# Kernel optimization log

Hardware: AMD Instinct MI355X
Metric: run time of the kernel (lower is better)

The kernel has to match this reference:

```python
import jax, jax.numpy as jnp
import numpy as np

_LARGE = 1e10
LN_EPS = 1e-12
K_TOP = 32
ROWS = 512


def setup_inputs() -> dict:
    key = jax.random.key(0)
    ks = jax.random.split(key, 12)
    B, T, H = 32, 128, 768
    M, D_KEY, D_VAL = 131072, 128, 512
    N = 1024  # n_mentions
    return {
        'encoding': jax.random.normal(ks[0], (B, T, H), jnp.float32),
        'mention_batch_positions': jax.random.randint(ks[1], (N,), 0, B),
        'mention_start_positions': jax.random.randint(ks[2], (N,), 0, T),
        'mention_end_positions': jax.random.randint(ks[3], (N,), 0, T),
        'mention_mask': jnp.ones((N,), jnp.float32),
        'memory_keys': jax.random.normal(ks[4], (M, D_KEY), jnp.float32),
        'memory_values': jax.random.normal(ks[5], (M, D_VAL), jnp.float32),
        'memory_mask': jax.random.randint(ks[6], (M,), 0, 2),
        'memory_entity_ids': jax.random.randint(ks[7], (M,), 0, 1000000),
        # learned params
        'query_w': jax.random.normal(ks[8], (2 * H, D_KEY), jnp.float32) * 0.02,
        'query_b': jnp.zeros((D_KEY,), jnp.float32),
        'update_w': jax.random.normal(ks[9], (D_VAL, H), jnp.float32) * 0.02,
        'update_b': jnp.zeros((H,), jnp.float32),
        'ln_scale': jnp.ones((H,), jnp.float32),
        'ln_bias': jnp.zeros((H,), jnp.float32),
        'deterministic': 1,
    }


def reference(encoding, mention_batch_positions, mention_start_positions,
              mention_end_positions, mention_mask, memory_keys, memory_values,
              memory_mask, memory_entity_ids, query_w, query_b, update_w,
              update_b, ln_scale, ln_bias, deterministic):
    M, d_key = memory_keys.shape
    vpr = M // ROWS  # values per row

    # gather mention boundary token encodings: [N, H] each
    start_enc = encoding[mention_batch_positions, mention_start_positions]
    end_enc = encoding[mention_batch_positions, mention_end_positions]
    queries = jnp.concatenate([start_enc, end_enc], axis=-1) @ query_w + query_b  # [N, d_key]

    # approximate top-k: top-1 per row, then top-k over row maxima
    table = memory_keys.reshape(ROWS, vpr, d_key)
    q_sg = jax.lax.stop_gradient(queries)
    scores = jnp.einsum('qd,rvd->qrv', q_sg, table)  # [N, ROWS, vpr]
    top_local_id = jnp.argmax(scores, axis=-1)       # [N, ROWS]
    top_row_score = jnp.max(scores, axis=-1)         # [N, ROWS]
    _, top_rows = jax.lax.top_k(top_row_score, K_TOP)  # [N, K]
    local = jnp.take_along_axis(top_local_id, top_rows, axis=-1)
    top_ids = top_rows * vpr + local                 # [N, K] global memory ids

    top_keys = memory_keys[top_ids]                  # [N, K, d_key]
    top_values = memory_values[top_ids]              # [N, K, d_val]
    top_entity_ids = memory_entity_ids[top_ids]      # [N, K]

    # rescore with-gradient and mask invalid memory slots
    top_scores = jnp.einsum('qd,qkd->qk', queries, top_keys)
    top_scores = top_scores - (1 - memory_mask[top_ids]).astype(top_scores.dtype) * _LARGE
    attention_weights = jax.nn.softmax(top_scores, axis=-1)  # [N, K]

    # additive retrieval update: pool, project, scatter-add at start pos, LN
    pooled = jnp.einsum('qk,qkd->qd', attention_weights, top_values)  # [N, d_val]
    projected = (pooled @ update_w + update_b) * mention_mask[:, None]  # [N, H]
    enc = encoding.at[mention_batch_positions, mention_start_positions].add(projected)
    mean = jnp.mean(enc, axis=-1, keepdims=True)
    var = jnp.var(enc, axis=-1, keepdims=True)
    enc = (enc - mean) / jnp.sqrt(var + LN_EPS) * ln_scale + ln_bias
    return enc, attention_weights, top_entity_ids
```

## Files before the change

### kernel.cpp

```cpp
#include <hip/hip_runtime.h>
#include <math.h>

#define B_ 32
#define T_ 128
#define H_ 768
#define N_ 1024
#define M_ 131072
#define DK 128
#define DV 512
#define NROWS 512
#define VPR 256
#define KTOP 32
#define EPS2 1.2f
#define CCAP 96

typedef __attribute__((ext_vector_type(8))) short short8v;
typedef __attribute__((ext_vector_type(4))) float f32x4;

#define WS_QF64   ((size_t)0)
#define WS_QHI    (WS_QF64 + (size_t)N_*DK*8)
#define WS_RMAX1  (WS_QHI + (size_t)N_*DK*2)
#define WS_RMAX2  (WS_RMAX1 + (size_t)N_*NROWS*4)
#define WS_RMAX3  (WS_RMAX2 + (size_t)N_*NROWS*4)
#define WS_POOLED (WS_RMAX3 + (size_t)N_*NROWS*4)
#define WS_DELTA  (WS_POOLED + (size_t)N_*DV*4)
#define WS_KHI    (WS_DELTA + (size_t)B_*T_*H_*4)

__device__ __forceinline__ unsigned short bf16_rn(float x) {
  unsigned u = __float_as_uint(x);
  unsigned r = u + 0x7FFFu + ((u >> 16) & 1u);
  return (unsigned short)(r >> 16);
}

__device__ __forceinline__ void gload16(const void* g, void* l) {
  __builtin_amdgcn_global_load_lds(
      (const __attribute__((address_space(1))) void*)g,
      (__attribute__((address_space(3))) void*)l, 16, 0, 0);
}

__device__ __forceinline__ void ins3(float p, float& v1, float& v2, float& v3) {
  float m1 = fminf(v1, p);
  v1 = fmaxf(v1, p);
  float m2 = fminf(v2, m1);
  v2 = fmaxf(v2, m1);
  v3 = fmaxf(v3, m2);
}

__global__ __launch_bounds__(256) void k_zero(float4* __restrict__ p) {
  p[(size_t)blockIdx.x * 256 + threadIdx.x] = (float4){0.f, 0.f, 0.f, 0.f};
}

__global__ __launch_bounds__(256) void k_split(
    const float* __restrict__ keys, unsigned short* __restrict__ khi) {
  int t = threadIdx.x;
  int key = blockIdx.x * 16 + (t >> 4);
  int gt = t & 15;
  const float* src = keys + (size_t)key * DK + gt * 8;
  float4 f0 = *(const float4*)(src);
  float4 f1 = *(const float4*)(src + 4);
  float f[8] = {f0.x, f0.y, f0.z, f0.w, f1.x, f1.y, f1.z, f1.w};
  unsigned h[8];
#pragma unroll
  for (int i = 0; i < 8; ++i) h[i] = bf16_rn(f[i]);
  int kir = key & 255, row = key >> 8;
  int g = gt ^ (kir & 15);
  size_t base = (size_t)row * 32768 + (size_t)kir * 128 + g * 8;
  uint4 uh = {h[0] | (h[1] << 16), h[2] | (h[3] << 16),
              h[4] | (h[5] << 16), h[6] | (h[7] << 16)};
  *(uint4*)(khi + base) = uh;
}

__global__ __launch_bounds__(512) void k_queries(
    const float* __restrict__ enc, const int* __restrict__ mbp,
    const int* __restrict__ msp, const int* __restrict__ mep,
    const float* __restrict__ qw, const float* __restrict__ qb,
    double* __restrict__ qf64, unsigned short* __restrict__ qhi) {
  int g = blockIdx.x, t = threadIdx.x;
  int d = t & 127, qq = t >> 7;
  __shared__ float se[4][H_], ee[4][H_];
  __shared__ double part[4][512];
#pragma unroll
  for (int mm = 0; mm < 4; ++mm) {
    int m = g * 4 + mm;
    int b = mbp[m], s = msp[m], e = mep[m];
    const float* rs = enc + ((size_t)(b * T_ + s)) * H_;
    const float* re = enc + ((size_t)(b * T_ + e)) * H_;
    for (int h = t; h < H_; h += 512) { se[mm][h] = rs[h]; ee[mm][h] = re[h]; }
  }
  __syncthreads();
  int h0 = (qq & 1) * 384;
  int wbase = (qq >> 1) * H_ + h0;
  double acc0 = 0, acc1 = 0, acc2 = 0, acc3 = 0;
  if (qq < 2) {
    for (int h = 0; h < 384; ++h) {
      double w = (double)qw[(size_t)(wbase + h) * DK + d];
      acc0 += (double)se[0][h0 + h] * w; acc1 += (double)se[1][h0 + h] * w;
      acc2 += (double)se[2][h0 + h] * w; acc3 += (double)se[3][h0 + h] * w;
    }
  } else {
    for (int h = 0; h < 384; ++h) {
      double w = (double)qw[(size_t)(wbase + h) * DK + d];
      acc0 += (double)ee[0][h0 + h] * w; acc1 += (double)ee[1][h0 + h] * w;
      acc2 += (double)ee[2][h0 + h] * w; acc3 += (double)ee[3][h0 + h] * w;
    }
  }
  part[0][t] = acc0; part[1][t] = acc1; part[2][t] = acc2; part[3][t] = acc3;
  __syncthreads();
  {
    int mm = t >> 7, dd = t & 127;
    int m = g * 4 + mm;
    double v = (double)qb[dd] + part[mm][dd] + part[mm][dd + 128] +
               part[mm][dd + 256] + part[mm][dd + 384];
    qf64[(size_t)m * DK + dd] = v;
    unsigned hv = bf16_rn((float)v);
    int mtg = m >> 4, r16 = m & 15, ks = dd >> 5, sub = (dd >> 3) & 3;
    size_t idx = ((size_t)(mtg * 4 + ks) * 64 + sub * 16 + r16) * 8 + (dd & 7);
    qhi[idx] = (unsigned short)hv;
  }
}

__global__ __launch_bounds__(512, 4) void k_score(
    const unsigned short* __restrict__ khi,
    const unsigned short* __restrict__ qhi,
    float* __restrict__ rmax1, float* __restrict__ rmax2,
    float* __restrict__ rmax3) {
  __shared__ unsigned short klds[4][32 * DK];
  __shared__ float mbuf[128][6];
  int id = blockIdx.x;
  int row = (id & 7) * 64 + (id >> 6);
  int Q = (id >> 3) & 7;
  int tid = threadIdx.x;
  int lane = tid & 63, wave = tid >> 6;
  int mg = wave >> 1, kg = wave & 1;
  int l15 = lane & 15, l4 = lane >> 4;

  const char* srcH = (const char*)khi + (size_t)row * 65536;

  auto stage = [&](int c, int buf) {
    int off = wave * 1024;
    gload16(srcH + c * 8192 + off + lane * 16, (char*)&klds[buf][0] + off);
  };

  short8v ah[4][2];
#pragma unroll
  for (int ks = 0; ks < 4; ++ks)
#pragma unroll
    for (int mt = 0; mt < 2; ++mt) {
      int mtg = Q * 8 + mg * 2 + mt;
      size_t aoff = ((size_t)(mtg * 4 + ks) * 64 + lane) * 8;
      ah[ks][mt] = *(const short8v*)(qhi + aoff);
    }

  float rv1[2][4], rv2[2][4], rv3[2][4];
#pragma unroll
  for (int mt = 0; mt < 2; ++mt)
#pragma unroll
    for (int r = 0; r < 4; ++r) {
      rv1[mt][r] = -INFINITY; rv2[mt][r] = -INFINITY; rv3[mt][r] = -INFINITY;
    }

  stage(0, 0);
  stage(1, 1);
  stage(2, 2);

#pragma unroll
  for (int c = 0; c < 8; ++c) {
    if (c < 6)      asm volatile("s_waitcnt vmcnt(2)" ::: "memory");
    else if (c < 7) asm volatile("s_waitcnt vmcnt(1)" ::: "memory");
    else            asm volatile("s_waitcnt vmcnt(0)" ::: "memory");
    __builtin_amdgcn_s_barrier();
    __builtin_amdgcn_sched_barrier(0);
    if (c < 5) stage(c + 3, (c + 3) & 3);
    int buf = c & 3;

    f32x4 acc[2];
    acc[0] = (f32x4){0.f, 0.f, 0.f, 0.f};
    acc[1] = (f32x4){0.f, 0.f, 0.f, 0.f};
    __builtin_amdgcn_s_setprio(1);
#pragma unroll
    for (int ks = 0; ks < 4; ++ks) {
      int kir = kg * 16 + l15;
      int off = kir * DK + (((l4 + 4 * ks) ^ l15) << 3);
      short8v bh = *(const short8v*)(&klds[buf][off]);
#pragma unroll
      for (int mt = 0; mt < 2; ++mt)
        acc[mt] = __builtin_amdgcn_mfma_f32_16x16x32_bf16(ah[ks][mt], bh, acc[mt], 0, 0, 0);
    }
    __builtin_amdgcn_s_setprio(0);

    unsigned idx = (unsigned)(c * 32 + kg * 16 + l15);
#pragma unroll
    for (int mt = 0; mt < 2; ++mt)
#pragma unroll
      for (int r = 0; r < 4; ++r) {
        float p = __uint_as_float((__float_as_uint(acc[mt][r]) & 0xFFFFFF00u) | idx);
        ins3(p, rv1[mt][r], rv2[mt][r], rv3[mt][r]);
      }
  }

#pragma unroll
  for (int mt = 0; mt < 2; ++mt)
#pragma unroll
    for (int r = 0; r < 4; ++r) {
      float v1 = rv1[mt][r], v2 = rv2[mt][r], v3 = rv3[mt][r];
#pragma unroll
      for (int s = 1; s < 16; s <<= 1) {
        float w1 = __shfl_xor(v1, s, 16);
        float w2 = __shfl_xor(v2, s, 16);
        float w3 = __shfl_xor(v3, s, 16);
        ins3(w1, v1, v2, v3);
        ins3(w2, v1, v2, v3);
        ins3(w3, v1, v2, v3);
      }
      if (l15 == 0) {
        int mloc = (mg * 2 + mt) * 16 + l4 * 4 + r;
        mbuf[mloc][kg * 3]     = v1;
        mbuf[mloc][kg * 3 + 1] = v2;
        mbuf[mloc][kg * 3 + 2] = v3;
      }
    }
  __syncthreads();

  if (tid < 128) {
    float v1 = mbuf[tid][0], v2 = mbuf[tid][1], v3 = mbuf[tid][2];
    ins3(mbuf[tid][3], v1, v2, v3);
    ins3(mbuf[tid][4], v1, v2, v3);
    ins3(mbuf[tid][5], v1, v2, v3);
    size_t o = (size_t)row * N_ + Q * 128 + tid;
    rmax1[o] = v1;
    rmax2[o] = v2;
    rmax3[o] = v3;
  }
}

__global__ __launch_bounds__(256) void k_select(
    const double* __restrict__ qf64, const float* __restrict__ keys,
    const float* __restrict__ rmax1, const float* __restrict__ rmax2,
    const float* __restrict__ rmax3,
    const int* __restrict__ memmask, const int* __restrict__ eids,
    const float* __restrict__ mvals,
    float* __restrict__ out_w, float* __restrict__ out_ids,
    float* __restrict__ pooled) {
  int m = blockIdx.x, tid = threadIdx.x;
  __shared__ double q_d[DK];
  __shared__ float  vals[NROWS];
  __shared__ unsigned long long skey[NROWS];
  __shared__ int    slotRow[CCAP];
  __shared__ float  slotV[CCAP];
  __shared__ double cval[CCAP];
  __shared__ int    carg[CCAP];
  __shared__ float  Tsh;
  __shared__ int    Csh;
  __shared__ int    fgid[KTOP];
  __shared__ double fval[KTOP];
  __shared__ float  wsm[KTOP];

  for (int i = tid; i < DK; i += 256) q_d[i] = qf64[(size_t)m * DK + i];
  for (int i = tid; i < NROWS; i += 256) {
    float v = rmax1[(size_t)i * N_ + m];
    vals[i] = v;
    unsigned u = __float_as_uint(v);
    unsigned ordv = (u & 0x80000000u) ? ~u : (u | 0x80000000u);
    skey[i] = ((unsigned long long)(~ordv) << 32) | (unsigned)i;
  }
  __syncthreads();

  for (int k = 2; k <= NROWS; k <<= 1) {
    for (int j = k >> 1; j > 0; j >>= 1) {
      for (int i = tid; i < NROWS; i += 256) {
        int p = i ^ j;
        if (p > i) {
          bool up = ((i & k) == 0);
          unsigned long long a = skey[i], b = skey[p];
          if ((a > b) == up) { skey[i] = b; skey[p] = a; }
        }
      }
      __syncthreads();
    }
  }

  if (tid < CCAP) {
    int r = (int)(skey[tid] & 0xFFFFFFFFu);
    slotRow[tid] = r;
    slotV[tid] = vals[r];
  }
  __syncthreads();
  if (tid == 0) {
    Tsh = slotV[KTOP - 1] - EPS2;
    int C = KTOP;
    while (C < CCAP && slotV[C] >= Tsh) ++C;
    Csh = C;
  }
  __syncthreads();
  int C = Csh;

  if (tid < C) {
    int row = slotRow[tid];
    size_t o = (size_t)row * N_ + m;
    float v1 = vals[row], v2 = rmax2[o], v3 = rmax3[o];
    int i1 = (int)(__float_as_uint(v1) & 0xFFu);
    int i2 = (int)(__float_as_uint(v2) & 0xFFu);
    int i3 = (int)(__float_as_uint(v3) & 0xFFu);
    const float* kp = keys + ((size_t)row * VPR + i1) * DK;
    double s1 = 0.0;
    for (int d = 0; d < DK; ++d) s1 += q_d[d] * (double)kp[d];
    double val = s1; int arg = i1;
    if (v1 - v2 <= EPS2) {
      const float* kp2 = keys + ((size_t)row * VPR + i2) * DK;
      double s2 = 0.0;
      for (int d = 0; d < DK; ++d) s2 += q_d[d] * (double)kp2[d];
      if (s2 > val || (s2 == val && i2 < arg)) { val = s2; arg = i2; }
    }
    if (v1 - v3 <= EPS2) {
      const float* kp3 = keys + ((size_t)row * VPR + i3) * DK;
      double s3 = 0.0;
      for (int d = 0; d < DK; ++d) s3 += q_d[d] * (double)kp3[d];
      if (s3 > val || (s3 == val && i3 < arg)) { val = s3; arg = i3; }
    }
    cval[tid] = val; carg[tid] = arg;
  }
  __syncthreads();

  if (tid < C) {
    double v = cval[tid]; int row = slotRow[tid]; int rank = 0;
    for (int j = 0; j < C; ++j) {
      double u = cval[j]; int rj = slotRow[j];
      rank += (u > v) | ((u == v) & (rj < row));
    }
    if (rank < KTOP) { fgid[rank] = row * VPR + carg[tid]; fval[rank] = v; }
  }
  __syncthreads();

  if (tid < KTOP) {
    int gid = fgid[tid];
    double sc = fval[tid] - (1.0 - (double)memmask[gid]) * 1e10;
    double mx = sc;
#pragma unroll
    for (int off = 16; off >= 1; off >>= 1) mx = fmax(mx, __shfl_xor(mx, off, 32));
    double e = exp(sc - mx), ss = e;
#pragma unroll
    for (int off = 16; off >= 1; off >>= 1) ss += __shfl_xor(ss, off, 32);
    float w = (float)(e / ss);
    out_w[(size_t)m * KTOP + tid] = w;
    out_ids[(size_t)m * KTOP + tid] = (float)eids[gid];
    wsm[tid] = w;
  }
  __syncthreads();

  for (int d = tid; d < DV; d += 256) {
    float acc = 0.f;
#pragma unroll 8
    for (int i = 0; i < KTOP; ++i) acc += wsm[i] * mvals[(size_t)fgid[i] * DV + d];
    pooled[(size_t)m * DV + d] = acc;
  }
}

__global__ __launch_bounds__(256) void k_project(
    const float* __restrict__ pooled, const float* __restrict__ uw,
    const float* __restrict__ ub, const float* __restrict__ mmsk,
    const int* __restrict__ mbp, const int* __restrict__ msp,
    float* __restrict__ delta) {
  int mt = blockIdx.x, tid = threadIdx.x;
  __shared__ float p_s[4 * DV];
  for (int i = tid; i < 4 * DV; i += 256) p_s[i] = pooled[(size_t)mt * 4 * DV + i];
  __syncthreads();
  float a0[4] = {}, a1[4] = {}, a2[4] = {};
  for (int d = 0; d < DV; ++d) {
    float w0 = uw[(size_t)d * H_ + tid];
    float w1 = uw[(size_t)d * H_ + tid + 256];
    float w2 = uw[(size_t)d * H_ + tid + 512];
#pragma unroll
    for (int q = 0; q < 4; ++q) {
      float p = p_s[q * DV + d];
      a0[q] += p * w0; a1[q] += p * w1; a2[q] += p * w2;
    }
  }
#pragma unroll
  for (int q = 0; q < 4; ++q) {
    int m = mt * 4 + q;
    float msk = mmsk[m];
    float* dst = delta + ((size_t)(mbp[m] * T_ + msp[m])) * H_;
    atomicAdd(dst + tid,       (a0[q] + ub[tid])       * msk);
    atomicAdd(dst + tid + 256, (a1[q] + ub[tid + 256]) * msk);
    atomicAdd(dst + tid + 512, (a2[q] + ub[tid + 512]) * msk);
  }
}

__device__ __forceinline__ float blockReduceSum(float v, float* red, int tid) {
#pragma unroll
  for (int off = 32; off >= 1; off >>= 1) v += __shfl_xor(v, off, 64);
  __syncthreads();
  if ((tid & 63) == 0) red[tid >> 6] = v;
  __syncthreads();
  return red[0] + red[1] + red[2] + red[3];
}

__global__ __launch_bounds__(256) void k_ln(
    const float* __restrict__ enc, const float* __restrict__ delta,
    const float* __restrict__ lns, const float* __restrict__ lnb,
    float* __restrict__ out) {
  int r = blockIdx.x, tid = threadIdx.x;
  size_t base = (size_t)r * H_;
  __shared__ float red[4];
  float x0 = enc[base + tid]       + delta[base + tid];
  float x1 = enc[base + tid + 256] + delta[base + tid + 256];
  float x2 = enc[base + tid + 512] + delta[base + tid + 512];
  float mu = blockReduceSum(x0 + x1 + x2, red, tid) * (1.f / 768.f);
  float d0 = x0 - mu, d1 = x1 - mu, d2 = x2 - mu;
  float var = blockReduceSum(d0 * d0 + d1 * d1 + d2 * d2, red, tid) * (1.f / 768.f);
  float rs = 1.f / sqrtf(var + 1e-12f);
  out[base + tid]       = d0 * rs * lns[tid]       + lnb[tid];
  out[base + tid + 256] = d1 * rs * lns[tid + 256] + lnb[tid + 256];
  out[base + tid + 512] = d2 * rs * lns[tid + 512] + lnb[tid + 512];
}

extern "C" void kernel_launch(void* const* d_in, const int* in_sizes, int n_in,
                              void* d_out, int out_size, void* d_ws, size_t ws_size,
                              hipStream_t stream) {
  (void)in_sizes; (void)n_in; (void)out_size; (void)ws_size;
  const float* enc     = (const float*)d_in[0];
  const int*   mbp     = (const int*)d_in[1];
  const int*   msp     = (const int*)d_in[2];
  const int*   mep     = (const int*)d_in[3];
  const float* mmsk    = (const float*)d_in[4];
  const float* keys    = (const float*)d_in[5];
  const float* mvals   = (const float*)d_in[6];
  const int*   memmask = (const int*)d_in[7];
  const int*   eids    = (const int*)d_in[8];
  const float* qw      = (const float*)d_in[9];
  const float* qb      = (const float*)d_in[10];
  const float* uw      = (const float*)d_in[11];
  const float* ub      = (const float*)d_in[12];
  const float* lns     = (const float*)d_in[13];
  const float* lnb     = (const float*)d_in[14];

  char* ws = (char*)d_ws;
  double*         qf64   = (double*)(ws + WS_QF64);
  unsigned short* qhi    = (unsigned short*)(ws + WS_QHI);
  float*          rmax1  = (float*)(ws + WS_RMAX1);
  float*          rmax2  = (float*)(ws + WS_RMAX2);
  float*          rmax3  = (float*)(ws + WS_RMAX3);
  float*          pooled = (float*)(ws + WS_POOLED);
  float*          delta  = (float*)(ws + WS_DELTA);
  unsigned short* khi    = (unsigned short*)(ws + WS_KHI);

  float* out_enc = (float*)d_out;
  float* out_w   = out_enc + (size_t)B_ * T_ * H_;
  float* out_ids = out_w + (size_t)N_ * KTOP;

  k_zero<<<(B_ * T_ * H_) / 1024, 256, 0, stream>>>((float4*)delta);
  k_split<<<M_ / 16, 256, 0, stream>>>(keys, khi);
  k_queries<<<N_ / 4, 512, 0, stream>>>(enc, mbp, msp, mep, qw, qb, qf64, qhi);
  k_score<<<NROWS * 8, 512, 0, stream>>>(khi, qhi, rmax1, rmax2, rmax3);
  k_select<<<N_, 256, 0, stream>>>(qf64, keys, rmax1, rmax2, rmax3,
                                   memmask, eids, mvals, out_w, out_ids, pooled);
  k_project<<<N_ / 4, 256, 0, stream>>>(pooled, uw, ub, mmsk, mbp, msp, delta);
  k_ln<<<B_ * T_, 256, 0, stream>>>(enc, delta, lns, lnb, out_enc);
}
```

Before: 239.3 us.

## Fuse key bf16 conversion into score kernel and fold zeroing into queries

The separate fp32-to-bf16 key split pass is removed. Each score block now converts its whole 256-key row into swizzled LDS once and loops over all 8 query groups, with keys as the MFMA A operand and queries as B. Delta zeroing moves into the queries kernel, dropping two launches and the khi workspace round trip. In exchange the grid shrinks from 4096 to 512 blocks, there is no async prefetch pipeline, LDS use per block grows to 64KB, and two barriers are added per query group, so occupancy and latency hiding may suffer.

```diff
diff --git a/kernel.cpp b/kernel.cpp
--- a/kernel.cpp
+++ b/kernel.cpp
@@ -24,18 +24,11 @@
 #define WS_RMAX3  (WS_RMAX2 + (size_t)N_*NROWS*4)
 #define WS_POOLED (WS_RMAX3 + (size_t)N_*NROWS*4)
 #define WS_DELTA  (WS_POOLED + (size_t)N_*DV*4)
-#define WS_KHI    (WS_DELTA + (size_t)B_*T_*H_*4)
 
 __device__ __forceinline__ unsigned short bf16_rn(float x) {
   unsigned u = __float_as_uint(x);
   unsigned r = u + 0x7FFFu + ((u >> 16) & 1u);
   return (unsigned short)(r >> 16);
-}
-
-__device__ __forceinline__ void gload16(const void* g, void* l) {
-  __builtin_amdgcn_global_load_lds(
-      (const __attribute__((address_space(1))) void*)g,
-      (__attribute__((address_space(3))) void*)l, 16, 0, 0);
 }
 
 __device__ __forceinline__ void ins3(float p, float& v1, float& v2, float& v3) {
@@ -46,36 +39,18 @@
   v3 = fmaxf(v3, m2);
 }
 
-__global__ __launch_bounds__(256) void k_zero(float4* __restrict__ p) {
-  p[(size_t)blockIdx.x * 256 + threadIdx.x] = (float4){0.f, 0.f, 0.f, 0.f};
-}
-
-__global__ __launch_bounds__(256) void k_split(
-    const float* __restrict__ keys, unsigned short* __restrict__ khi) {
-  int t = threadIdx.x;
-  int key = blockIdx.x * 16 + (t >> 4);
-  int gt = t & 15;
-  const float* src = keys + (size_t)key * DK + gt * 8;
-  float4 f0 = *(const float4*)(src);
-  float4 f1 = *(const float4*)(src + 4);
-  float f[8] = {f0.x, f0.y, f0.z, f0.w, f1.x, f1.y, f1.z, f1.w};
-  unsigned h[8];
-#pragma unroll
-  for (int i = 0; i < 8; ++i) h[i] = bf16_rn(f[i]);
-  int kir = key & 255, row = key >> 8;
-  int g = gt ^ (kir & 15);
-  size_t base = (size_t)row * 32768 + (size_t)kir * 128 + g * 8;
-  uint4 uh = {h[0] | (h[1] << 16), h[2] | (h[3] << 16),
-              h[4] | (h[5] << 16), h[6] | (h[7] << 16)};
-  *(uint4*)(khi + base) = uh;
-}
-
 __global__ __launch_bounds__(512) void k_queries(
     const float* __restrict__ enc, const int* __restrict__ mbp,
     const int* __restrict__ msp, const int* __restrict__ mep,
     const float* __restrict__ qw, const float* __restrict__ qb,
-    double* __restrict__ qf64, unsigned short* __restrict__ qhi) {
+    double* __restrict__ qf64, unsigned short* __restrict__ qhi,
+    float4* __restrict__ delta4) {
   int g = blockIdx.x, t = threadIdx.x;
+  {
+    size_t zb = (size_t)g * 3072 + t;
+#pragma unroll
+    for (int j = 0; j < 6; ++j) delta4[zb + j * 512] = (float4){0.f, 0.f, 0.f, 0.f};
+  }
   int d = t & 127, qq = t >> 7;
   __shared__ float se[4][H_], ee[4][H_];
   __shared__ double part[4][512];
@@ -120,116 +95,108 @@
 }
 
 __global__ __launch_bounds__(512, 4) void k_score(
-    const unsigned short* __restrict__ khi,
-    const unsigned short* __restrict__ qhi,
+    const float* __restrict__ keys, const unsigned short* __restrict__ qhi,
     float* __restrict__ rmax1, float* __restrict__ rmax2,
     float* __restrict__ rmax3) {
-  __shared__ unsigned short klds[4][32 * DK];
+  __shared__ unsigned short klds[VPR * DK];
   __shared__ float mbuf[128][6];
-  int id = blockIdx.x;
-  int row = (id & 7) * 64 + (id >> 6);
-  int Q = (id >> 3) & 7;
+  int row = blockIdx.x;
   int tid = threadIdx.x;
   int lane = tid & 63, wave = tid >> 6;
   int mg = wave >> 1, kg = wave & 1;
   int l15 = lane & 15, l4 = lane >> 4;
 
-  const char* srcH = (const char*)khi + (size_t)row * 65536;
-
-  auto stage = [&](int c, int buf) {
-    int off = wave * 1024;
-    gload16(srcH + c * 8192 + off + lane * 16, (char*)&klds[buf][0] + off);
-  };
-
-  short8v ah[4][2];
-#pragma unroll
-  for (int ks = 0; ks < 4; ++ks)
+  {
+    int key = tid >> 1, half = tid & 1;
+    const float* src = keys + ((size_t)row * VPR + key) * DK + half * 64;
+    int swz = key & 15;
+#pragma unroll
+    for (int j = 0; j < 8; ++j) {
+      float4 fa = *(const float4*)(src + j * 8);
+      float4 fb = *(const float4*)(src + j * 8 + 4);
+      unsigned h0 = (unsigned)bf16_rn(fa.x) | ((unsigned)bf16_rn(fa.y) << 16);
+      unsigned h1 = (unsigned)bf16_rn(fa.z) | ((unsigned)bf16_rn(fa.w) << 16);
+      unsigned h2 = (unsigned)bf16_rn(fb.x) | ((unsigned)bf16_rn(fb.y) << 16);
+      unsigned h3 = (unsigned)bf16_rn(fb.z) | ((unsigned)bf16_rn(fb.w) << 16);
+      int gg = (half * 8 + j) ^ swz;
+      uint4 u = {h0, h1, h2, h3};
+      *(uint4*)(&klds[key * DK + (gg << 3)]) = u;
+    }
+  }
+  __syncthreads();
+
+  for (int Q = 0; Q < 8; ++Q) {
+    short8v bq[4][2];
+#pragma unroll
+    for (int ks = 0; ks < 4; ++ks)
+#pragma unroll
+      for (int mt = 0; mt < 2; ++mt) {
+        int mtg = Q * 8 + mg * 2 + mt;
+        size_t aoff = ((size_t)(mtg * 4 + ks) * 64 + lane) * 8;
+        bq[ks][mt] = *(const short8v*)(qhi + aoff);
+      }
+
+    float rv1[2], rv2[2], rv3[2];
 #pragma unroll
     for (int mt = 0; mt < 2; ++mt) {
-      int mtg = Q * 8 + mg * 2 + mt;
-      size_t aoff = ((size_t)(mtg * 4 + ks) * 64 + lane) * 8;
-      ah[ks][mt] = *(const short8v*)(qhi + aoff);
-    }
-
-  float rv1[2][4], rv2[2][4], rv3[2][4];
-#pragma unroll
-  for (int mt = 0; mt < 2; ++mt)
-#pragma unroll
-    for (int r = 0; r < 4; ++r) {
-      rv1[mt][r] = -INFINITY; rv2[mt][r] = -INFINITY; rv3[mt][r] = -INFINITY;
-    }
-
-  stage(0, 0);
-  stage(1, 1);
-  stage(2, 2);
-
-#pragma unroll
-  for (int c = 0; c < 8; ++c) {
-    if (c < 6)      asm volatile("s_waitcnt vmcnt(2)" ::: "memory");
-    else if (c < 7) asm volatile("s_waitcnt vmcnt(1)" ::: "memory");
-    else            asm volatile("s_waitcnt vmcnt(0)" ::: "memory");
-    __builtin_amdgcn_s_barrier();
-    __builtin_amdgcn_sched_barrier(0);
-    if (c < 5) stage(c + 3, (c + 3) & 3);
-    int buf = c & 3;
-
-    f32x4 acc[2];
-    acc[0] = (f32x4){0.f, 0.f, 0.f, 0.f};
-    acc[1] = (f32x4){0.f, 0.f, 0.f, 0.f};
-    __builtin_amdgcn_s_setprio(1);
-#pragma unroll
-    for (int ks = 0; ks < 4; ++ks) {
-      int kir = kg * 16 + l15;
-      int off = kir * DK + (((l4 + 4 * ks) ^ l15) << 3);
-      short8v bh = *(const short8v*)(&klds[buf][off]);
+      rv1[mt] = -INFINITY; rv2[mt] = -INFINITY; rv3[mt] = -INFINITY;
+    }
+
+#pragma unroll
+    for (int kt = 0; kt < 8; ++kt) {
+      f32x4 acc[2];
+      acc[0] = (f32x4){0.f, 0.f, 0.f, 0.f};
+      acc[1] = (f32x4){0.f, 0.f, 0.f, 0.f};
+#pragma unroll
+      for (int ks = 0; ks < 4; ++ks) {
+        int kir = kg * 128 + kt * 16 + l15;
+        int off = kir * DK + (((l4 + 4 * ks) ^ l15) << 3);
+        short8v ak = *(const short8v*)(&klds[off]);
+        acc[0] = __builtin_amdgcn_mfma_f32_16x16x32_bf16(ak, bq[ks][0], acc[0], 0, 0, 0);
+        acc[1] = __builtin_amdgcn_mfma_f32_16x16x32_bf16(ak, bq[ks][1], acc[1], 0, 0, 0);
+      }
 #pragma unroll
       for (int mt = 0; mt < 2; ++mt)
-        acc[mt] = __builtin_amdgcn_mfma_f32_16x16x32_bf16(ah[ks][mt], bh, acc[mt], 0, 0, 0);
-    }
-    __builtin_amdgcn_s_setprio(0);
-
-    unsigned idx = (unsigned)(c * 32 + kg * 16 + l15);
-#pragma unroll
-    for (int mt = 0; mt < 2; ++mt)
-#pragma unroll
-      for (int r = 0; r < 4; ++r) {
-        float p = __uint_as_float((__float_as_uint(acc[mt][r]) & 0xFFFFFF00u) | idx);
-        ins3(p, rv1[mt][r], rv2[mt][r], rv3[mt][r]);
-      }
-  }
-
-#pragma unroll
-  for (int mt = 0; mt < 2; ++mt)
-#pragma unroll
-    for (int r = 0; r < 4; ++r) {
-      float v1 = rv1[mt][r], v2 = rv2[mt][r], v3 = rv3[mt][r];
-#pragma unroll
-      for (int s = 1; s < 16; s <<= 1) {
-        float w1 = __shfl_xor(v1, s, 16);
-        float w2 = __shfl_xor(v2, s, 16);
-        float w3 = __shfl_xor(v3, s, 16);
+#pragma unroll
+        for (int r = 0; r < 4; ++r) {
+          unsigned kidx = (unsigned)(kg * 128 + kt * 16 + l4 * 4 + r);
+          float p = __uint_as_float((__float_as_uint(acc[mt][r]) & 0xFFFFFF00u) | kidx);
+          ins3(p, rv1[mt], rv2[mt], rv3[mt]);
+        }
+    }
+
+#pragma unroll
+    for (int mt = 0; mt < 2; ++mt) {
+      float v1 = rv1[mt], v2 = rv2[mt], v3 = rv3[mt];
+#pragma unroll
+      for (int s = 16; s <= 32; s <<= 1) {
+        float w1 = __shfl_xor(v1, s, 64);
+        float w2 = __shfl_xor(v2, s, 64);
+        float w3 = __shfl_xor(v3, s, 64);
         ins3(w1, v1, v2, v3);
         ins3(w2, v1, v2, v3);
         ins3(w3, v1, v2, v3);
       }
-      if (l15 == 0) {
-        int mloc = (mg * 2 + mt) * 16 + l4 * 4 + r;
+      if (l4 == 0) {
+        int mloc = mg * 32 + mt * 16 + l15;
         mbuf[mloc][kg * 3]     = v1;
         mbuf[mloc][kg * 3 + 1] = v2;
         mbuf[mloc][kg * 3 + 2] = v3;
       }
     }
-  __syncthreads();
-
-  if (tid < 128) {
-    float v1 = mbuf[tid][0], v2 = mbuf[tid][1], v3 = mbuf[tid][2];
-    ins3(mbuf[tid][3], v1, v2, v3);
-    ins3(mbuf[tid][4], v1, v2, v3);
-    ins3(mbuf[tid][5], v1, v2, v3);
-    size_t o = (size_t)row * N_ + Q * 128 + tid;
-    rmax1[o] = v1;
-    rmax2[o] = v2;
-    rmax3[o] = v3;
+    __syncthreads();
+
+    if (tid < 128) {
+      float v1 = mbuf[tid][0], v2 = mbuf[tid][1], v3 = mbuf[tid][2];
+      ins3(mbuf[tid][3], v1, v2, v3);
+      ins3(mbuf[tid][4], v1, v2, v3);
+      ins3(mbuf[tid][5], v1, v2, v3);
+      size_t o = (size_t)row * N_ + Q * 128 + tid;
+      rmax1[o] = v1;
+      rmax2[o] = v2;
+      rmax3[o] = v3;
+    }
+    __syncthreads();
   }
 }
 
@@ -442,16 +409,14 @@
   float*          rmax3  = (float*)(ws + WS_RMAX3);
   float*          pooled = (float*)(ws + WS_POOLED);
   float*          delta  = (float*)(ws + WS_DELTA);
-  unsigned short* khi    = (unsigned short*)(ws + WS_KHI);
 
   float* out_enc = (float*)d_out;
   float* out_w   = out_enc + (size_t)B_ * T_ * H_;
   float* out_ids = out_w + (size_t)N_ * KTOP;
 
-  k_zero<<<(B_ * T_ * H_) / 1024, 256, 0, stream>>>((float4*)delta);
-  k_split<<<M_ / 16, 256, 0, stream>>>(keys, khi);
-  k_queries<<<N_ / 4, 512, 0, stream>>>(enc, mbp, msp, mep, qw, qb, qf64, qhi);
-  k_score<<<NROWS * 8, 512, 0, stream>>>(khi, qhi, rmax1, rmax2, rmax3);
+  k_queries<<<N_ / 4, 512, 0, stream>>>(enc, mbp, msp, mep, qw, qb, qf64, qhi,
+                                        (float4*)delta);
+  k_score<<<NROWS, 512, 0, stream>>>(keys, qhi, rmax1, rmax2, rmax3);
   k_select<<<N_, 256, 0, stream>>>(qf64, keys, rmax1, rmax2, rmax3,
                                    memmask, eids, mvals, out_w, out_ids, pooled);
   k_project<<<N_ / 4, 256, 0, stream>>>(pooled, uw, ub, mmsk, mbp, msp, delta);
```

Measured after the change: 193.4 us. 19.2% less time.
